# Kernel optimization log

Hardware: AMD Instinct MI355X
Metric: run time of the kernel (lower is better)

## Reference

```python
import jax, jax.numpy as jnp
import numpy as np
import math

B, L, D, MAXL = 4, 4096, 1024, 16384


def setup_inputs() -> dict:
    key = jax.random.key(0)
    ks = jax.random.split(key, 12)
    s = 0.02
    def w(k, shape):
        return jax.random.normal(k, shape, jnp.float32) * s
    return {
        "x": jax.random.normal(ks[0], (B, L, D), jnp.float32),
        "pos_phases": jax.random.normal(ks[1], (MAXL, D), jnp.float32) * math.pi,
        "Wpv": w(ks[2], (D, D)), "bpv": jnp.zeros((D,), jnp.float32),
        "Wk": w(ks[3], (D, D)), "bk": jnp.zeros((D,), jnp.float32),
        "Wkv": w(ks[4], (D, D)), "bkv": jnp.zeros((D,), jnp.float32),
        "Wg1": w(ks[5], (2 * D, D)), "bg1": jnp.zeros((D,), jnp.float32),
        "Wg2": w(ks[6], (D, 1)), "bg2": jnp.zeros((1,), jnp.float32),
        "Wb1": w(ks[7], (D, D // 2)), "bb1": jnp.zeros((D // 2,), jnp.float32),
        "Wb2": w(ks[8], (D // 2, 2)), "bb2": jnp.zeros((2,), jnp.float32),
        "ln_g": jnp.ones((D,), jnp.float32), "ln_b": jnp.zeros((D,), jnp.float32),
        "Wo": w(ks[9], (D, D)), "bo": jnp.zeros((D,), jnp.float32),
    }


def _shift1(a):
    # torch.roll(a, 1, dims=1) with a[:, 0] = 0
    return jnp.concatenate([jnp.zeros_like(a[:, :1]), a[:, :-1]], axis=1)


def reference(x, pos_phases, Wpv, bpv, Wk, bk, Wkv, bkv, Wg1, bg1, Wg2, bg2,
              Wb1, bb1, Wb2, bb2, ln_g, ln_b, Wo, bo):
    Bq, Lq, Dq = x.shape
    sqrtD = jnp.sqrt(jnp.float32(Dq))

    # positional phasor memory
    pp = pos_phases[:Lq]                      # [L, D]
    pos_cos, pos_sin = jnp.cos(pp), jnp.sin(pp)
    pos_values = x @ Wpv + bpv                # [B, L, D]
    pos_mem_cos = jnp.cumsum(pos_cos * pos_values, axis=1)
    pos_mem_sin = jnp.cumsum(pos_sin * pos_values, axis=1)
    pos_ret = (pos_cos * pos_mem_cos + pos_sin * pos_mem_sin) / sqrtD

    # key-value phasor memory
    key_ph = jnp.tanh(x @ Wk + bk) * jnp.pi
    key_cos, key_sin = jnp.cos(key_ph), jnp.sin(key_ph)
    kv_values = x @ Wkv + bkv

    x_shifted = _shift1(x)
    gate_in = jnp.concatenate([x, x_shifted], axis=-1)       # [B, L, 2D]
    gh = jax.nn.gelu(gate_in @ Wg1 + bg1, approximate=False)
    value_gates = jax.nn.sigmoid(gh @ Wg2 + bg2)             # [B, L, 1]

    kc_s = _shift1(key_cos)
    ks_s = _shift1(key_sin)
    kv_mem_cos = jnp.cumsum(kc_s * kv_values * value_gates, axis=1)
    kv_mem_sin = jnp.cumsum(ks_s * kv_values * value_gates, axis=1)
    gate_cumsum = jnp.maximum(jnp.cumsum(value_gates, axis=1), 1.0)
    kv_ret = (key_cos * kv_mem_cos + key_sin * kv_mem_sin) / (jnp.sqrt(gate_cumsum) * sqrtD)

    # blend
    bh = jax.nn.gelu(x @ Wb1 + bb1, approximate=False)
    bw = jax.nn.softmax(bh @ Wb2 + bb2, axis=-1)             # [B, L, 2]
    blended = bw[..., 0:1] * pos_ret + bw[..., 1:2] * kv_ret

    # to_out: LayerNorm then Linear
    mu = jnp.mean(blended, axis=-1, keepdims=True)
    var = jnp.var(blended, axis=-1, keepdims=True)
    ln = (blended - mu) / jnp.sqrt(var + 1e-5) * ln_g + ln_b
    return x + ln @ Wo + bo
```

## Files before the change

kernel.cpp:

```cpp
#include <hip/hip_runtime.h>
#include <hip/hip_bf16.h>
#include <math.h>

using bf16 = __hip_bfloat16;
typedef __bf16 v8bf __attribute__((ext_vector_type(8)));
typedef float v4f __attribute__((ext_vector_type(4)));

#define B_ 4
#define L_ 4096
#define D_ 1024
#define M_ (B_*L_)
#define CCH 128
#define LCH (L_/CCH)
#define NF 3584

__device__ __forceinline__ float bf2f(bf16 v){ return __bfloat162float(v); }
__device__ __forceinline__ bf16 f2bf(float v){ return __float2bfloat16(v); }
__device__ __forceinline__ float us2f(ushort u){ union{unsigned u32; float f;}c; c.u32=((unsigned)u)<<16; return c.f; }
__device__ __forceinline__ ushort f2us(float v){ bf16 h=__float2bfloat16(v); return *(ushort*)&h; }
__device__ __forceinline__ float h2f(ushort u){ union{ushort s; _Float16 h;}c; c.s=u; return (float)c.h; }
__device__ __forceinline__ ushort f2h(float v){ union{ushort s; _Float16 h;}c; c.h=(_Float16)v; return c.s; }

__device__ __forceinline__ void g2l16(const void* g, void* l){
  __builtin_amdgcn_global_load_lds(
    (const __attribute__((address_space(1))) unsigned int*)g,
    (__attribute__((address_space(3))) unsigned int*)l, 16, 0, 0);
}

__global__ void k_zeroN(float* __restrict__ p, int n){
  int i = blockIdx.x*256 + threadIdx.x;
  if (i < n) p[i] = 0.0f;
}

__global__ void k_cvt(const float* __restrict__ in, bf16* __restrict__ out){
  int i = (blockIdx.x*256 + threadIdx.x)*4;
  float4 v = *(const float4*)(in + i);
  out[i]   = f2bf(v.x);
  out[i+1] = f2bf(v.y);
  out[i+2] = f2bf(v.z);
  out[i+3] = f2bf(v.w);
}

__global__ void k_cvt_pp(const float* __restrict__ in, ushort* __restrict__ out){
  int i = (blockIdx.x*256 + threadIdx.x)*4;
  float4 v = *(const float4*)(in + i);
  out[i]   = f2h(v.x);
  out[i+1] = f2h(v.y);
  out[i+2] = f2h(v.z);
  out[i+3] = f2h(v.w);
}

__global__ void k_ctr(const float* __restrict__ in, bf16* __restrict__ out, int R, int C){
  __shared__ float tile[32][33];
  int c0 = blockIdx.x*32, r0 = blockIdx.y*32;
  #pragma unroll
  for (int i=0;i<32;i+=8)
    tile[threadIdx.y+i][threadIdx.x] = in[(size_t)(r0+threadIdx.y+i)*C + c0+threadIdx.x];
  __syncthreads();
  #pragma unroll
  for (int i=0;i<32;i+=8)
    out[(size_t)(c0+threadIdx.y+i)*R + r0+threadIdx.x] = f2bf(tile[threadIdx.x][threadIdx.y+i]);
}

__global__ void k_pack_bias(const float* __restrict__ bpv, const float* __restrict__ bk,
                            const float* __restrict__ bkv, const float* __restrict__ bb1,
                            float* __restrict__ bf){
  int i = blockIdx.x*256 + threadIdx.x;
  float v;
  if (i < 1024) v = bpv[i];
  else if (i < 2048) v = bk[i-1024];
  else if (i < 3072) v = bkv[i-2048];
  else v = bb1[i-3072];
  bf[i] = v;
}

__device__ __forceinline__ float geluf(float v){
  return 0.5f*v*(1.0f + erff(v*0.70710678118654752f));
}
__device__ __forceinline__ float fast_tanh(float v){
  float a = fabsf(v);
  float e = __expf(-2.0f*a);
  float t = (1.0f - e)/(1.0f + e);
  return copysignf(t, v);
}

#define BM 128
#define BN 128
#define BK 32

template<int EPI, bool CONCAT>
__global__ __launch_bounds__(256) void k_gemm(
    const bf16* __restrict__ A, int lda,
    const bf16* __restrict__ Bt, int ldb,
    const float* __restrict__ bias,
    const bf16* __restrict__ zeros,
    bf16* __restrict__ o_pv, ushort* __restrict__ o_kp, bf16* __restrict__ o_kv,
    const float* __restrict__ Wv2, const float* __restrict__ Wb2f,
    float* __restrict__ gaccp, float* __restrict__ bwaccp,
    float* __restrict__ outf, const float* __restrict__ residf,
    int N, int Ktot)
{
  __shared__ __align__(16) ushort As[BM*BK];
  __shared__ __align__(16) ushort Bs[BN*BK];
  int tid = threadIdx.x;
  int lane = tid & 63, wave = tid >> 6;
  int wm = wave & 1, wn = wave >> 1;
  int bn = blockIdx.x * BN, bm = blockIdx.y * BM;

  v4f zero = {0.f,0.f,0.f,0.f};
  v4f acc[4][4];
  #pragma unroll
  for (int i=0;i<4;i++)
    #pragma unroll
    for (int j=0;j<4;j++) acc[i][j] = zero;

  int sub = lane >> 2;
  int seg = lane & 3;
  int mr = lane & 15, g4 = lane >> 4;

  auto mfma_step = [&](){
    v8bf af[4], bfr[4];
    #pragma unroll
    for (int i=0;i<4;i++) af[i]  = *(const v8bf*)&As[(wm*64 + i*16 + mr)*BK + g4*8];
    #pragma unroll
    for (int j=0;j<4;j++) bfr[j] = *(const v8bf*)&Bs[(wn*64 + j*16 + mr)*BK + g4*8];
    #pragma unroll
    for (int i=0;i<4;i++)
      #pragma unroll
      for (int j=0;j<4;j++)
        acc[i][j] = __builtin_amdgcn_mfma_f32_16x16x32_bf16(af[i], bfr[j], acc[i][j], 0, 0, 0);
  };
  auto stage_b = [&](int kk){
    #pragma unroll
    for (int s=0;s<2;s++){
      int q = wave*2 + s;
      int row = q*16 + sub;
      g2l16(Bt + (size_t)(bn+row)*ldb + (size_t)kk + seg*8, Bs + q*512);
    }
  };

  int k1 = CONCAT ? D_ : Ktot;
  for (int kk = 0; kk < k1; kk += BK) {
    #pragma unroll
    for (int s=0;s<2;s++){
      int q = wave*2 + s;
      int row = q*16 + sub;
      g2l16(A + (size_t)(bm+row)*lda + (size_t)kk + seg*8, As + q*512);
    }
    stage_b(kk);
    __syncthreads();
    mfma_step();
    __syncthreads();
  }
  if (CONCAT){
    for (int kk = D_; kk < Ktot; kk += BK) {
      #pragma unroll
      for (int s=0;s<2;s++){
        int q = wave*2 + s;
        int row = q*16 + sub;
        int m = bm + row;
        int l = m & (L_-1);
        const bf16* src = (l==0) ? (zeros + seg*8)
                                 : (A + (size_t)(m-1)*lda + (size_t)(kk - D_) + seg*8);
        g2l16(src, As + q*512);
      }
      stage_b(kk);
      __syncthreads();
      mfma_step();
      __syncthreads();
    }
  }

  int lr = lane >> 4, lc = lane & 15;
  if (EPI == 3){
    #pragma unroll
    for (int i=0;i<4;i++){
      #pragma unroll
      for (int j=0;j<4;j++){
        int col  = bn + wn*64 + j*16 + lc;
        int row0 = bm + wm*64 + i*16 + lr*4;
        float bias_v = bias[col];
        #pragma unroll
        for (int rr=0; rr<4; rr++){
          size_t idx = (size_t)(row0+rr)*N + col;
          outf[idx] = acc[i][j][rr] + bias_v + residf[idx];
        }
      }
    }
  } else if (EPI == 2){
    #pragma unroll
    for (int i=0;i<4;i++){
      float red[4] = {0.f,0.f,0.f,0.f};
      #pragma unroll
      for (int j=0;j<4;j++){
        int col = bn + wn*64 + j*16 + lc;
        float bias_v = bias[col];
        float wv = Wv2[col];
        #pragma unroll
        for (int rr=0; rr<4; rr++){
          float v = acc[i][j][rr] + bias_v;
          red[rr] += geluf(v) * wv;
        }
      }
      int row0 = bm + wm*64 + i*16 + lr*4;
      #pragma unroll
      for (int rr=0; rr<4; rr++){
        float r = red[rr];
        r += __shfl_xor(r,1); r += __shfl_xor(r,2);
        r += __shfl_xor(r,4); r += __shfl_xor(r,8);
        if (lc == 0) atomicAdd(&gaccp[row0+rr], r);
      }
    }
  } else {
    if (bn < 3072){
      #pragma unroll
      for (int i=0;i<4;i++){
        #pragma unroll
        for (int j=0;j<4;j++){
          int col  = bn + wn*64 + j*16 + lc;
          int row0 = bm + wm*64 + i*16 + lr*4;
          float bias_v = bias[col];
          #pragma unroll
          for (int rr=0; rr<4; rr++){
            int row = row0 + rr;
            float v = acc[i][j][rr] + bias_v;
            if (bn < 1024) {
              o_pv[(size_t)row*1024 + col] = f2bf(v);
            } else if (bn < 2048) {
              float kp = fast_tanh(v) * 3.14159265358979323846f;
              o_kp[(size_t)row*1024 + (col-1024)] = f2h(kp);
            } else {
              o_kv[(size_t)row*1024 + (col-2048)] = f2bf(v);
            }
          }
        }
      }
    } else {
      #pragma unroll
      for (int i=0;i<4;i++){
        float r0[4] = {0.f,0.f,0.f,0.f};
        float r1[4] = {0.f,0.f,0.f,0.f};
        #pragma unroll
        for (int j=0;j<4;j++){
          int col = bn + wn*64 + j*16 + lc;
          float bias_v = bias[col];
          int kb = col - 3072;
          float w0 = Wb2f[kb*2], w1 = Wb2f[kb*2+1];
          #pragma unroll
          for (int rr=0; rr<4; rr++){
            float v = acc[i][j][rr] + bias_v;
            float gl = geluf(v);
            r0[rr] += gl*w0;
            r1[rr] += gl*w1;
          }
        }
        int row0 = bm + wm*64 + i*16 + lr*4;
        #pragma unroll
        for (int rr=0; rr<4; rr++){
          float a = r0[rr], b = r1[rr];
          a += __shfl_xor(a,1); a += __shfl_xor(a,2); a += __shfl_xor(a,4); a += __shfl_xor(a,8);
          b += __shfl_xor(b,1); b += __shfl_xor(b,2); b += __shfl_xor(b,4); b += __shfl_xor(b,8);
          if (lc == 0){
            atomicAdd(&bwaccp[(size_t)(row0+rr)*2],   a);
            atomicAdd(&bwaccp[(size_t)(row0+rr)*2+1], b);
          }
        }
      }
    }
  }
}

__global__ __launch_bounds__(1024) void k_gscan(const float* __restrict__ gacc,
                                                const float* __restrict__ bg2,
                                                float* __restrict__ g, float* __restrict__ gc){
  __shared__ float sa[1024];
  int b = blockIdx.x, tid = threadIdx.x;
  int base = b*L_ + tid*4;
  float bb = bg2[0];
  float v0 = 1.f/(1.f+__expf(-(gacc[base]   + bb)));
  float v1 = 1.f/(1.f+__expf(-(gacc[base+1] + bb)));
  float v2 = 1.f/(1.f+__expf(-(gacc[base+2] + bb)));
  float v3 = 1.f/(1.f+__expf(-(gacc[base+3] + bb)));
  float s0 = v0, s1 = s0+v1, s2 = s1+v2, s3 = s2+v3;
  sa[tid] = s3; __syncthreads();
  for (int o=1;o<1024;o<<=1){
    float t = sa[tid] + ((tid>=o) ? sa[tid-o] : 0.f);
    __syncthreads();
    sa[tid] = t;
    __syncthreads();
  }
  float ex = sa[tid] - s3;
  g[base]=v0; g[base+1]=v1; g[base+2]=v2; g[base+3]=v3;
  gc[base]=ex+s0; gc[base+1]=ex+s1; gc[base+2]=ex+s2; gc[base+3]=ex+s3;
}

__global__ void k_finishbw(const float* __restrict__ bwacc, const float* __restrict__ bb2,
                           float2* __restrict__ bw){
  int t = blockIdx.x*256 + threadIdx.x;
  float a = bwacc[(size_t)t*2]   + bb2[0];
  float b = bwacc[(size_t)t*2+1] + bb2[1];
  float m = fmaxf(a,b);
  float e0 = __expf(a-m), e1 = __expf(b-m);
  float inv = 1.0f/(e0+e1);
  bw[t] = make_float2(e0*inv, e1*inv);
}

__global__ void k_scan_partial(const bf16* __restrict__ PV, const bf16* __restrict__ KV,
                               const ushort* __restrict__ KP, const float* __restrict__ g,
                               const ushort* __restrict__ ppH, float* __restrict__ PS){
  int tid = threadIdx.x;
  int d0 = tid*4;
  int j = blockIdx.x, b = blockIdx.y;
  int l0 = j*LCH;
  float pkc[4]={0,0,0,0}, pks[4]={0,0,0,0};
  if (l0 > 0){
    size_t pidx = ((size_t)b*L_ + l0-1)*D_ + d0;
    ushort4 up = *(const ushort4*)(KP+pidx);
    float ph0=h2f(up.x), ph1=h2f(up.y), ph2=h2f(up.z), ph3=h2f(up.w);
    __sincosf(ph0,&pks[0],&pkc[0]); __sincosf(ph1,&pks[1],&pkc[1]);
    __sincosf(ph2,&pks[2],&pkc[2]); __sincosf(ph3,&pks[3],&pkc[3]);
  }
  float p0[4]={0,0,0,0}, p1[4]={0,0,0,0}, p2[4]={0,0,0,0}, p3[4]={0,0,0,0};
  for (int l=l0; l<l0+LCH; l++){
    size_t idx = ((size_t)b*L_ + l)*D_ + d0;
    ushort4 upv = *(const ushort4*)(PV+idx);
    ushort4 ukv = *(const ushort4*)(KV+idx);
    ushort4 ukp = *(const ushort4*)(KP+idx);
    ushort4 upp = *(const ushort4*)(ppH + (size_t)l*D_ + d0);
    float gl = g[b*L_ + l];
    float pvv[4]={us2f(upv.x),us2f(upv.y),us2f(upv.z),us2f(upv.w)};
    float kvv[4]={us2f(ukv.x),us2f(ukv.y),us2f(ukv.z),us2f(ukv.w)};
    float kpv[4]={h2f(ukp.x),h2f(ukp.y),h2f(ukp.z),h2f(ukp.w)};
    float phv[4]={h2f(upp.x),h2f(upp.y),h2f(upp.z),h2f(upp.w)};
    #pragma unroll
    for (int c=0;c<4;c++){
      float sn, cs; __sincosf(phv[c], &sn, &cs);
      float kc, ks; __sincosf(kpv[c], &ks, &kc);
      float kvg = kvv[c]*gl;
      p0[c] += cs*pvv[c]; p1[c] += sn*pvv[c];
      p2[c] += pkc[c]*kvg; p3[c] += pks[c]*kvg;
      pkc[c]=kc; pks[c]=ks;
    }
  }
  size_t base = ((size_t)b*CCH + j)*D_ + d0;
  size_t plane = (size_t)B_*CCH*D_;
  #pragma unroll
  for (int c=0;c<4;c++){
    PS[0*plane + base + c] = p0[c];
    PS[1*plane + base + c] = p1[c];
    PS[2*plane + base + c] = p2[c];
    PS[3*plane + base + c] = p3[c];
  }
}

__global__ void k_prefix(float* __restrict__ PS){
  int idx = blockIdx.x*256 + threadIdx.x;
  int q = idx >> 12;
  int rem = idx & 4095;
  int b = rem >> 10, d = rem & 1023;
  size_t plane = (size_t)B_*CCH*D_;
  float* base = PS + (size_t)q*plane + (size_t)b*CCH*D_ + d;
  float s = 0.0f;
  for (int j=0;j<CCH;j+=4){
    float v0 = base[(size_t)(j  )*D_];
    float v1 = base[(size_t)(j+1)*D_];
    float v2 = base[(size_t)(j+2)*D_];
    float v3 = base[(size_t)(j+3)*D_];
    base[(size_t)(j  )*D_] = s; s += v0;
    base[(size_t)(j+1)*D_] = s; s += v1;
    base[(size_t)(j+2)*D_] = s; s += v2;
    base[(size_t)(j+3)*D_] = s; s += v3;
  }
}

__global__ void k_scan_apply(const bf16* __restrict__ PV, const bf16* __restrict__ KV,
                             const ushort* __restrict__ KP, const float* __restrict__ g,
                             const ushort* __restrict__ ppH, const float* __restrict__ PS,
                             const float* __restrict__ gc, const float2* __restrict__ bw,
                             const float* __restrict__ ln_g, const float* __restrict__ ln_b,
                             bf16* __restrict__ LNB){
  __shared__ float sA[4], sB[4];
  int tid = threadIdx.x;
  int d0 = tid*4;
  int j = blockIdx.x, b = blockIdx.y;
  int l0 = j*LCH;
  size_t base = ((size_t)b*CCH + j)*D_ + d0;
  size_t plane = (size_t)B_*CCH*D_;
  float mc[4], ms[4], kcm[4], ksm[4];
  #pragma unroll
  for (int c=0;c<4;c++){
    mc[c]  = PS[0*plane+base+c]; ms[c]  = PS[1*plane+base+c];
    kcm[c] = PS[2*plane+base+c]; ksm[c] = PS[3*plane+base+c];
  }
  float pkc[4]={0,0,0,0}, pks[4]={0,0,0,0};
  if (l0 > 0){
    size_t pidx = ((size_t)b*L_ + l0-1)*D_ + d0;
    ushort4 up = *(const ushort4*)(KP+pidx);
    float ph0=h2f(up.x), ph1=h2f(up.y), ph2=h2f(up.z), ph3=h2f(up.w);
    __sincosf(ph0,&pks[0],&pkc[0]); __sincosf(ph1,&pks[1],&pkc[1]);
    __sincosf(ph2,&pks[2],&pkc[2]); __sincosf(ph3,&pks[3],&pkc[3]);
  }
  float4 gv = *(const float4*)&ln_g[d0];
  float4 bv = *(const float4*)&ln_b[d0];
  int wv = tid >> 6, ln = tid & 63;
  for (int l=l0; l<l0+LCH; l++){
    size_t idx = ((size_t)b*L_ + l)*D_ + d0;
    ushort4 upv = *(const ushort4*)(PV+idx);
    ushort4 ukv = *(const ushort4*)(KV+idx);
    ushort4 ukp = *(const ushort4*)(KP+idx);
    ushort4 upp = *(const ushort4*)(ppH + (size_t)l*D_ + d0);
    float gl = g[b*L_ + l];
    float gcv = fmaxf(gc[b*L_+l], 1.0f);
    float rs = 0.03125f * rsqrtf(gcv);
    float2 w = bw[b*L_+l];
    float pvv[4]={us2f(upv.x),us2f(upv.y),us2f(upv.z),us2f(upv.w)};
    float kvv[4]={us2f(ukv.x),us2f(ukv.y),us2f(ukv.z),us2f(ukv.w)};
    float kpv[4]={h2f(ukp.x),h2f(ukp.y),h2f(ukp.z),h2f(ukp.w)};
    float phv[4]={h2f(upp.x),h2f(upp.y),h2f(upp.z),h2f(upp.w)};
    float bl[4];
    #pragma unroll
    for (int c=0;c<4;c++){
      float sn, cs; __sincosf(phv[c], &sn, &cs);
      float kc, ks; __sincosf(kpv[c], &ks, &kc);
      mc[c] += cs*pvv[c]; ms[c] += sn*pvv[c];
      float pos_ret = (cs*mc[c] + sn*ms[c]) * 0.03125f;
      float kvg = kvv[c]*gl;
      kcm[c] += pkc[c]*kvg; ksm[c] += pks[c]*kvg;
      float kv_ret = (kc*kcm[c] + ks*ksm[c]) * rs;
      bl[c] = w.x*pos_ret + w.y*kv_ret;
      pkc[c]=kc; pks[c]=ks;
    }
    float s  = bl[0]+bl[1]+bl[2]+bl[3];
    float s2 = bl[0]*bl[0]+bl[1]*bl[1]+bl[2]*bl[2]+bl[3]*bl[3];
    #pragma unroll
    for (int o=1;o<64;o<<=1){ s += __shfl_xor(s,o); s2 += __shfl_xor(s2,o); }
    if (ln == 0){ sA[wv] = s; sB[wv] = s2; }
    __syncthreads();
    float ts  = sA[0]+sA[1]+sA[2]+sA[3];
    float ts2 = sB[0]+sB[1]+sB[2]+sB[3];
    __syncthreads();
    float mu   = ts * (1.0f/D_);
    float var  = ts2 * (1.0f/D_) - mu*mu;
    float rstd = rsqrtf(var + 1e-5f);
    ushort4 ou;
    ou.x = f2us((bl[0]-mu)*rstd*gv.x + bv.x);
    ou.y = f2us((bl[1]-mu)*rstd*gv.y + bv.y);
    ou.z = f2us((bl[2]-mu)*rstd*gv.z + bv.z);
    ou.w = f2us((bl[3]-mu)*rstd*gv.w + bv.w);
    *(ushort4*)((ushort*)LNB + idx) = ou;
  }
}

extern "C" void kernel_launch(void* const* d_in, const int* in_sizes, int n_in,
                              void* d_out, int out_size, void* d_ws, size_t ws_size,
                              hipStream_t stream) {
  const float* x     = (const float*)d_in[0];
  const float* phases= (const float*)d_in[1];
  const float* Wpv   = (const float*)d_in[2];
  const float* bpv   = (const float*)d_in[3];
  const float* Wk    = (const float*)d_in[4];
  const float* bk    = (const float*)d_in[5];
  const float* Wkv   = (const float*)d_in[6];
  const float* bkv   = (const float*)d_in[7];
  const float* Wg1   = (const float*)d_in[8];
  const float* bg1   = (const float*)d_in[9];
  const float* Wg2   = (const float*)d_in[10];
  const float* bg2   = (const float*)d_in[11];
  const float* Wb1   = (const float*)d_in[12];
  const float* bb1   = (const float*)d_in[13];
  const float* Wb2   = (const float*)d_in[14];
  const float* bb2   = (const float*)d_in[15];
  const float* ln_g  = (const float*)d_in[16];
  const float* ln_b  = (const float*)d_in[17];
  const float* Wo    = (const float*)d_in[18];
  const float* bo    = (const float*)d_in[19];
  float* out = (float*)d_out;

  char* ws = (char*)d_ws;
  size_t off = 0;
  auto alloc = [&](size_t bytes)->char*{
    char* p = ws + off; off += (bytes + 255) & ~(size_t)255; return p;
  };
  bf16*  xb   = (bf16*)alloc((size_t)M_*D_*2);
  bf16*  WfT  = (bf16*)alloc((size_t)NF*D_*2);
  bf16*  Wg1T = (bf16*)alloc((size_t)D_*2*D_*2);
  bf16*  WoT  = (bf16*)alloc((size_t)D_*D_*2);
  bf16*  PV   = (bf16*)alloc((size_t)M_*D_*2);
  bf16*  KV   = (bf16*)alloc((size_t)M_*D_*2);
  ushort* KP  = (ushort*)alloc((size_t)M_*D_*2);
  ushort* ppH = (ushort*)alloc((size_t)L_*D_*2);
  bf16*  LNB  = (bf16*)alloc((size_t)M_*D_*2);
  float* gbuf  = (float*)alloc((size_t)M_*4);
  float* gcbuf = (float*)alloc((size_t)M_*4);
  float2* bwbuf= (float2*)alloc((size_t)M_*8);
  float* PS    = (float*)alloc((size_t)4*B_*CCH*D_*4);
  float* biasF = (float*)alloc((size_t)NF*4);
  float* gacc  = (float*)alloc((size_t)M_*4);
  float* bwacc = (float*)alloc((size_t)M_*2*4);
  bf16*  zeros = (bf16*)alloc(256);
  int nzero = (M_ + 2*M_ + 64);

  k_zeroN<<<(nzero+255)/256,256,0,stream>>>(gacc, nzero);
  k_cvt<<<(M_*D_)/1024, 256, 0, stream>>>(x, xb);
  k_cvt_pp<<<(L_*D_)/1024, 256, 0, stream>>>(phases, ppH);

  dim3 tb(32,8);
  k_ctr<<<dim3(D_/32, D_/32), tb, 0, stream>>>(Wpv, WfT,                       D_, D_);
  k_ctr<<<dim3(D_/32, D_/32), tb, 0, stream>>>(Wk,  WfT + (size_t)1024*D_,     D_, D_);
  k_ctr<<<dim3(D_/32, D_/32), tb, 0, stream>>>(Wkv, WfT + (size_t)2048*D_,     D_, D_);
  k_ctr<<<dim3((D_/2)/32, D_/32), tb, 0, stream>>>(Wb1, WfT + (size_t)3072*D_, D_, D_/2);
  k_ctr<<<dim3(D_/32, 2*D_/32), tb, 0, stream>>>(Wg1, Wg1T, 2*D_, D_);
  k_ctr<<<dim3(D_/32, D_/32), tb, 0, stream>>>(Wo,  WoT,  D_, D_);
  k_pack_bias<<<NF/256,256,0,stream>>>(bpv, bk, bkv, bb1, biasF);

  k_gemm<4,false><<<dim3(NF/BN, M_/BM),256,0,stream>>>(
      xb, D_, WfT, D_, biasF, zeros, PV, KP, KV, nullptr, Wb2, nullptr, bwacc,
      nullptr, nullptr, NF, D_);
  k_gemm<2,true><<<dim3(D_/BN, M_/BM),256,0,stream>>>(
      xb, D_, Wg1T, 2*D_, bg1, zeros, nullptr, nullptr, nullptr, Wg2, nullptr, gacc, nullptr,
      nullptr, nullptr, D_, 2*D_);
  k_gscan<<<B_,1024,0,stream>>>(gacc, bg2, gbuf, gcbuf);
  k_finishbw<<<M_/256,256,0,stream>>>(bwacc, bb2, bwbuf);
  dim3 sg(CCH, B_);
  k_scan_partial<<<sg,256,0,stream>>>(PV, KV, KP, gbuf, ppH, PS);
  k_prefix<<<(4*B_*D_)/256,256,0,stream>>>(PS);
  k_scan_apply<<<sg,256,0,stream>>>(PV, KV, KP, gbuf, ppH, PS, gcbuf, bwbuf, ln_g, ln_b, LNB);
  k_gemm<3,false><<<dim3(D_/BN, M_/BM),256,0,stream>>>(
      LNB, D_, WoT, D_, bo, zeros, nullptr, nullptr, nullptr, nullptr, nullptr, nullptr, nullptr,
      out, x, D_, D_);
}
```

Before: 707.5 us.

## Enlarge GEMM tiles to 256x256x64 and double-buffer LDS staging

The bf16 MFMA GEMM kernel moves from 128x128x32 tiles with 256 threads to 256x256x64 tiles with 512 threads. Each wave now computes a 128x64 sub-tile. Global-to-LDS loads for the next K step are issued into a second buffer while the current buffer is computed, with explicit vmcnt waits and barriers. The goal is more data reuse per load and hiding global load latency. In exchange the kernel uses 128KB of LDS per block and many more accumulator registers, which lowers occupancy, and the grids get fewer blocks (NF=3584/256=14 columns, for example).

```diff
diff --git a/kernel.cpp b/kernel.cpp
--- a/kernel.cpp
+++ b/kernel.cpp
@@ -84,12 +84,12 @@
   return copysignf(t, v);
 }
 
-#define BM 128
-#define BN 128
-#define BK 32
+#define BM 256
+#define BN 256
+#define BK 64
 
 template<int EPI, bool CONCAT>
-__global__ __launch_bounds__(256) void k_gemm(
+__global__ __launch_bounds__(512) void k_gemm(
     const bf16* __restrict__ A, int lda,
     const bf16* __restrict__ Bt, int ldb,
     const float* __restrict__ bias,
@@ -100,85 +100,90 @@
     float* __restrict__ outf, const float* __restrict__ residf,
     int N, int Ktot)
 {
-  __shared__ __align__(16) ushort As[BM*BK];
-  __shared__ __align__(16) ushort Bs[BN*BK];
+  __shared__ __align__(16) ushort As[2*BM*BK];
+  __shared__ __align__(16) ushort Bs[2*BN*BK];
   int tid = threadIdx.x;
   int lane = tid & 63, wave = tid >> 6;
-  int wm = wave & 1, wn = wave >> 1;
+  int wm = wave >> 2, wn = wave & 3;
   int bn = blockIdx.x * BN, bm = blockIdx.y * BM;
 
   v4f zero = {0.f,0.f,0.f,0.f};
-  v4f acc[4][4];
+  v4f acc[8][4];
   #pragma unroll
-  for (int i=0;i<4;i++)
+  for (int i=0;i<8;i++)
     #pragma unroll
     for (int j=0;j<4;j++) acc[i][j] = zero;
 
-  int sub = lane >> 2;
-  int seg = lane & 3;
   int mr = lane & 15, g4 = lane >> 4;
-
-  auto mfma_step = [&](){
-    v8bf af[4], bfr[4];
-    #pragma unroll
-    for (int i=0;i<4;i++) af[i]  = *(const v8bf*)&As[(wm*64 + i*16 + mr)*BK + g4*8];
-    #pragma unroll
-    for (int j=0;j<4;j++) bfr[j] = *(const v8bf*)&Bs[(wn*64 + j*16 + mr)*BK + g4*8];
-    #pragma unroll
-    for (int i=0;i<4;i++)
-      #pragma unroll
-      for (int j=0;j<4;j++)
-        acc[i][j] = __builtin_amdgcn_mfma_f32_16x16x32_bf16(af[i], bfr[j], acc[i][j], 0, 0, 0);
+  int srow = lane >> 3, sseg = lane & 7;
+
+  auto stage = [&](int t, int buf){
+    int kk = t*BK;
+    ushort* Ad = As + buf*(BM*BK);
+    ushort* Bd = Bs + buf*(BN*BK);
+    #pragma unroll
+    for (int p=0;p<4;p++){
+      int r = p*64 + wave*8 + srow;
+      const bf16* src;
+      if (!CONCAT || kk < D_) {
+        src = A + (size_t)(bm + r)*lda + (size_t)kk + sseg*8;
+      } else {
+        int m = bm + r;
+        int l = m & (L_-1);
+        src = (l==0) ? (zeros + sseg*8)
+                     : (A + (size_t)(m-1)*lda + (size_t)(kk - D_) + sseg*8);
+      }
+      g2l16(src, Ad + (size_t)(p*64 + wave*8)*BK);
+    }
+    #pragma unroll
+    for (int p=0;p<4;p++){
+      int r = p*64 + wave*8 + srow;
+      g2l16(Bt + (size_t)(bn + r)*ldb + (size_t)kk + sseg*8,
+            Bd + (size_t)(p*64 + wave*8)*BK);
+    }
   };
-  auto stage_b = [&](int kk){
-    #pragma unroll
-    for (int s=0;s<2;s++){
-      int q = wave*2 + s;
-      int row = q*16 + sub;
-      g2l16(Bt + (size_t)(bn+row)*ldb + (size_t)kk + seg*8, Bs + q*512);
+
+  auto compute = [&](int buf){
+    const ushort* Ab = As + buf*(BM*BK);
+    const ushort* Bb = Bs + buf*(BN*BK);
+    #pragma unroll
+    for (int ks=0; ks<2; ks++){
+      v8bf a[8], b[4];
+      #pragma unroll
+      for (int i=0;i<8;i++) a[i] = *(const v8bf*)&Ab[(wm*128 + i*16 + mr)*BK + ks*32 + g4*8];
+      #pragma unroll
+      for (int j=0;j<4;j++) b[j] = *(const v8bf*)&Bb[(wn*64  + j*16 + mr)*BK + ks*32 + g4*8];
+      #pragma unroll
+      for (int i=0;i<8;i++)
+        #pragma unroll
+        for (int j=0;j<4;j++)
+          acc[i][j] = __builtin_amdgcn_mfma_f32_16x16x32_bf16(a[i], b[j], acc[i][j], 0, 0, 0);
     }
   };
 
-  int k1 = CONCAT ? D_ : Ktot;
-  for (int kk = 0; kk < k1; kk += BK) {
-    #pragma unroll
-    for (int s=0;s<2;s++){
-      int q = wave*2 + s;
-      int row = q*16 + sub;
-      g2l16(A + (size_t)(bm+row)*lda + (size_t)kk + seg*8, As + q*512);
-    }
-    stage_b(kk);
-    __syncthreads();
-    mfma_step();
-    __syncthreads();
-  }
-  if (CONCAT){
-    for (int kk = D_; kk < Ktot; kk += BK) {
-      #pragma unroll
-      for (int s=0;s<2;s++){
-        int q = wave*2 + s;
-        int row = q*16 + sub;
-        int m = bm + row;
-        int l = m & (L_-1);
-        const bf16* src = (l==0) ? (zeros + seg*8)
-                                 : (A + (size_t)(m-1)*lda + (size_t)(kk - D_) + seg*8);
-        g2l16(src, As + q*512);
-      }
-      stage_b(kk);
-      __syncthreads();
-      mfma_step();
-      __syncthreads();
-    }
+  int nt = Ktot / BK;
+  stage(0, 0);
+  for (int t=0; t<nt; ++t){
+    if (t+1 < nt){
+      stage(t+1, (t+1)&1);
+      asm volatile("s_waitcnt vmcnt(8)" ::: "memory");
+    } else {
+      asm volatile("s_waitcnt vmcnt(0)" ::: "memory");
+    }
+    asm volatile("s_barrier" ::: "memory");
+    compute(t&1);
+    asm volatile("s_waitcnt lgkmcnt(0)" ::: "memory");
+    asm volatile("s_barrier" ::: "memory");
   }
 
   int lr = lane >> 4, lc = lane & 15;
   if (EPI == 3){
     #pragma unroll
-    for (int i=0;i<4;i++){
+    for (int i=0;i<8;i++){
       #pragma unroll
       for (int j=0;j<4;j++){
         int col  = bn + wn*64 + j*16 + lc;
-        int row0 = bm + wm*64 + i*16 + lr*4;
+        int row0 = bm + wm*128 + i*16 + lr*4;
         float bias_v = bias[col];
         #pragma unroll
         for (int rr=0; rr<4; rr++){
@@ -189,7 +194,7 @@
     }
   } else if (EPI == 2){
     #pragma unroll
-    for (int i=0;i<4;i++){
+    for (int i=0;i<8;i++){
       float red[4] = {0.f,0.f,0.f,0.f};
       #pragma unroll
       for (int j=0;j<4;j++){
@@ -202,7 +207,7 @@
           red[rr] += geluf(v) * wv;
         }
       }
-      int row0 = bm + wm*64 + i*16 + lr*4;
+      int row0 = bm + wm*128 + i*16 + lr*4;
       #pragma unroll
       for (int rr=0; rr<4; rr++){
         float r = red[rr];
@@ -214,11 +219,11 @@
   } else {
     if (bn < 3072){
       #pragma unroll
-      for (int i=0;i<4;i++){
+      for (int i=0;i<8;i++){
         #pragma unroll
         for (int j=0;j<4;j++){
           int col  = bn + wn*64 + j*16 + lc;
-          int row0 = bm + wm*64 + i*16 + lr*4;
+          int row0 = bm + wm*128 + i*16 + lr*4;
           float bias_v = bias[col];
           #pragma unroll
           for (int rr=0; rr<4; rr++){
@@ -237,7 +242,7 @@
       }
     } else {
       #pragma unroll
-      for (int i=0;i<4;i++){
+      for (int i=0;i<8;i++){
         float r0[4] = {0.f,0.f,0.f,0.f};
         float r1[4] = {0.f,0.f,0.f,0.f};
         #pragma unroll
@@ -254,7 +259,7 @@
             r1[rr] += gl*w1;
           }
         }
-        int row0 = bm + wm*64 + i*16 + lr*4;
+        int row0 = bm + wm*128 + i*16 + lr*4;
         #pragma unroll
         for (int rr=0; rr<4; rr++){
           float a = r0[rr], b = r1[rr];
@@ -513,10 +518,10 @@
   k_ctr<<<dim3(D_/32, D_/32), tb, 0, stream>>>(Wo,  WoT,  D_, D_);
   k_pack_bias<<<NF/256,256,0,stream>>>(bpv, bk, bkv, bb1, biasF);
 
-  k_gemm<4,false><<<dim3(NF/BN, M_/BM),256,0,stream>>>(
+  k_gemm<4,false><<<dim3(NF/BN, M_/BM),512,0,stream>>>(
       xb, D_, WfT, D_, biasF, zeros, PV, KP, KV, nullptr, Wb2, nullptr, bwacc,
       nullptr, nullptr, NF, D_);
-  k_gemm<2,true><<<dim3(D_/BN, M_/BM),256,0,stream>>>(
+  k_gemm<2,true><<<dim3(D_/BN, M_/BM),512,0,stream>>>(
       xb, D_, Wg1T, 2*D_, bg1, zeros, nullptr, nullptr, nullptr, Wg2, nullptr, gacc, nullptr,
       nullptr, nullptr, D_, 2*D_);
   k_gscan<<<B_,1024,0,stream>>>(gacc, bg2, gbuf, gcbuf);
@@ -525,7 +530,7 @@
   k_scan_partial<<<sg,256,0,stream>>>(PV, KV, KP, gbuf, ppH, PS);
   k_prefix<<<(4*B_*D_)/256,256,0,stream>>>(PS);
   k_scan_apply<<<sg,256,0,stream>>>(PV, KV, KP, gbuf, ppH, PS, gcbuf, bwbuf, ln_g, ln_b, LNB);
-  k_gemm<3,false><<<dim3(D_/BN, M_/BM),256,0,stream>>>(
+  k_gemm<3,false><<<dim3(D_/BN, M_/BM),512,0,stream>>>(
       LNB, D_, WoT, D_, bo, zeros, nullptr, nullptr, nullptr, nullptr, nullptr, nullptr, nullptr,
       out, x, D_, D_);
 }
```

Result: faster. 661.1 us (-6.6%).

## Deepen GEMM K-tile with XOR-swizzled LDS, XCD-aware block remap and MFMA priority

Applied to the files above, without the earlier changes.

The GEMM K tile doubles to 64, so each barrier pair covers twice the MFMA work. The LDS layout gets an XOR swizzle to avoid bank conflicts on the wider rows. Workgroup IDs are remapped so consecutive tiles spread across the 8 XCDs for better L2 locality. MFMA bursts are wrapped in s_setprio, and the concat path merges into a single loop. The cost is more LDS per block, which may lower occupancy, plus more complex address math.

```diff
diff --git a/kernel.cpp b/kernel.cpp
--- a/kernel.cpp
+++ b/kernel.cpp
@@ -86,7 +86,7 @@
 
 #define BM 128
 #define BN 128
-#define BK 32
+#define BK 64
 
 template<int EPI, bool CONCAT>
 __global__ __launch_bounds__(256) void k_gemm(
@@ -104,8 +104,12 @@
   __shared__ __align__(16) ushort Bs[BN*BK];
   int tid = threadIdx.x;
   int lane = tid & 63, wave = tid >> 6;
-  int wm = wave & 1, wn = wave >> 1;
-  int bn = blockIdx.x * BN, bm = blockIdx.y * BM;
+  int wm = wave >> 1, wn = wave & 1;
+  int nwgx = gridDim.x;
+  int flat = blockIdx.y * nwgx + blockIdx.x;
+  int chunk = (nwgx * gridDim.y) >> 3;
+  int newid = (flat & 7) * chunk + (flat >> 3);
+  int bn = (newid % nwgx) * BN, bm = (newid / nwgx) * BM;
 
   v4f zero = {0.f,0.f,0.f,0.f};
   v4f acc[4][4];
@@ -114,61 +118,65 @@
     #pragma unroll
     for (int j=0;j<4;j++) acc[i][j] = zero;
 
-  int sub = lane >> 2;
-  int seg = lane & 3;
   int mr = lane & 15, g4 = lane >> 4;
-
-  auto mfma_step = [&](){
-    v8bf af[4], bfr[4];
-    #pragma unroll
-    for (int i=0;i<4;i++) af[i]  = *(const v8bf*)&As[(wm*64 + i*16 + mr)*BK + g4*8];
-    #pragma unroll
-    for (int j=0;j<4;j++) bfr[j] = *(const v8bf*)&Bs[(wn*64 + j*16 + mr)*BK + g4*8];
-    #pragma unroll
-    for (int i=0;i<4;i++)
-      #pragma unroll
-      for (int j=0;j<4;j++)
-        acc[i][j] = __builtin_amdgcn_mfma_f32_16x16x32_bf16(af[i], bfr[j], acc[i][j], 0, 0, 0);
+  int srow = lane >> 3, sseg = lane & 7;
+  int swzs = (sseg ^ srow) * 8;
+
+  auto stage_all = [&](int t){
+    int kk = t * BK;
+    #pragma unroll
+    for (int p=0;p<4;p++){
+      int r = p*32 + wave*8 + srow;
+      const bf16* src;
+      if (!CONCAT || kk < D_) {
+        src = A + (size_t)(bm + r)*lda + (size_t)kk + swzs;
+      } else {
+        int m = bm + r;
+        int l = m & (L_-1);
+        src = (l==0) ? (zeros + swzs)
+                     : (A + (size_t)(m-1)*lda + (size_t)(kk - D_) + swzs);
+      }
+      g2l16(src, As + (size_t)(p*32 + wave*8)*BK);
+    }
+    #pragma unroll
+    for (int p=0;p<4;p++){
+      int r = p*32 + wave*8 + srow;
+      g2l16(Bt + (size_t)(bn + r)*ldb + (size_t)kk + swzs,
+            Bs + (size_t)(p*32 + wave*8)*BK);
+    }
   };
-  auto stage_b = [&](int kk){
-    #pragma unroll
-    for (int s=0;s<2;s++){
-      int q = wave*2 + s;
-      int row = q*16 + sub;
-      g2l16(Bt + (size_t)(bn+row)*ldb + (size_t)kk + seg*8, Bs + q*512);
-    }
+
+  auto lds_a = [&](int i, int ks)->v8bf{
+    int row = wm*64 + i*16 + mr;
+    int off = row*128 + ((ks*64 + g4*16) ^ ((mr&7)<<4));
+    return *(const v8bf*)((const char*)As + off);
   };
-
-  int k1 = CONCAT ? D_ : Ktot;
-  for (int kk = 0; kk < k1; kk += BK) {
-    #pragma unroll
-    for (int s=0;s<2;s++){
-      int q = wave*2 + s;
-      int row = q*16 + sub;
-      g2l16(A + (size_t)(bm+row)*lda + (size_t)kk + seg*8, As + q*512);
-    }
-    stage_b(kk);
+  auto lds_b = [&](int j, int ks)->v8bf{
+    int row = wn*64 + j*16 + mr;
+    int off = row*128 + ((ks*64 + g4*16) ^ ((mr&7)<<4));
+    return *(const v8bf*)((const char*)Bs + off);
+  };
+
+  int nt = Ktot / BK;
+  for (int t=0; t<nt; ++t){
+    stage_all(t);
     __syncthreads();
-    mfma_step();
+    #pragma unroll
+    for (int ks=0; ks<2; ks++){
+      v8bf a[4], b[4];
+      #pragma unroll
+      for (int i=0;i<4;i++) a[i] = lds_a(i,ks);
+      #pragma unroll
+      for (int j=0;j<4;j++) b[j] = lds_b(j,ks);
+      __builtin_amdgcn_s_setprio(1);
+      #pragma unroll
+      for (int i=0;i<4;i++)
+        #pragma unroll
+        for (int j=0;j<4;j++)
+          acc[i][j] = __builtin_amdgcn_mfma_f32_16x16x32_bf16(a[i], b[j], acc[i][j], 0,0,0);
+      __builtin_amdgcn_s_setprio(0);
+    }
     __syncthreads();
-  }
-  if (CONCAT){
-    for (int kk = D_; kk < Ktot; kk += BK) {
-      #pragma unroll
-      for (int s=0;s<2;s++){
-        int q = wave*2 + s;
-        int row = q*16 + sub;
-        int m = bm + row;
-        int l = m & (L_-1);
-        const bf16* src = (l==0) ? (zeros + seg*8)
-                                 : (A + (size_t)(m-1)*lda + (size_t)(kk - D_) + seg*8);
-        g2l16(src, As + q*512);
-      }
-      stage_b(kk);
-      __syncthreads();
-      mfma_step();
-      __syncthreads();
-    }
   }
 
   int lr = lane >> 4, lc = lane & 15;
@@ -257,12 +265,12 @@
         int row0 = bm + wm*64 + i*16 + lr*4;
         #pragma unroll
         for (int rr=0; rr<4; rr++){
-          float a = r0[rr], b = r1[rr];
-          a += __shfl_xor(a,1); a += __shfl_xor(a,2); a += __shfl_xor(a,4); a += __shfl_xor(a,8);
-          b += __shfl_xor(b,1); b += __shfl_xor(b,2); b += __shfl_xor(b,4); b += __shfl_xor(b,8);
+          float a2 = r0[rr], b2 = r1[rr];
+          a2 += __shfl_xor(a2,1); a2 += __shfl_xor(a2,2); a2 += __shfl_xor(a2,4); a2 += __shfl_xor(a2,8);
+          b2 += __shfl_xor(b2,1); b2 += __shfl_xor(b2,2); b2 += __shfl_xor(b2,4); b2 += __shfl_xor(b2,8);
           if (lc == 0){
-            atomicAdd(&bwaccp[(size_t)(row0+rr)*2],   a);
-            atomicAdd(&bwaccp[(size_t)(row0+rr)*2+1], b);
+            atomicAdd(&bwaccp[(size_t)(row0+rr)*2],   a2);
+            atomicAdd(&bwaccp[(size_t)(row0+rr)*2+1], b2);
           }
         }
       }
```

After: 636.3 us. -10.1%, faster.
